# Kernel tuning notes

Hardware: AMD Instinct MI355X
Metric: run time of the kernel (lower is better)

Reference implementation:

```python
import jax, jax.numpy as jnp
import numpy as np
from jax.scipy.special import logsumexp

K, D, H, A = 8, 512, 512, 1024
S, T = 64, 128
B = S * T


def setup_inputs() -> dict:
    key = jax.random.key(0)
    k1, k2, k3, k4 = jax.random.split(key, 4)
    obs = jax.random.normal(k1, (B, D), dtype=jnp.float32)
    actions = jax.random.randint(k2, (B,), 0, A, dtype=jnp.int64)
    # uniform mixture prior (log(1/K)) => all components supported
    start_mixture_logprobs = jnp.full((S, K), jnp.log(1.0 / K), dtype=jnp.float32)
    W1 = jax.random.normal(k3, (K, D, H), dtype=jnp.float32) * 0.02
    b1 = jnp.zeros((K, H), dtype=jnp.float32)
    W2 = jax.random.normal(k4, (K, H, A), dtype=jnp.float32) * 0.02
    b2 = jnp.zeros((K, A), dtype=jnp.float32)
    return {"obs": obs, "actions": actions,
            "start_mixture_logprobs": start_mixture_logprobs,
            "W1": W1, "b1": b1, "W2": W2, "b2": b2, "seq_len": T}


def reference(obs, actions, start_mixture_logprobs, W1, b1, W2, b2, seq_len):
    num_seqs, num_comp = start_mixture_logprobs.shape
    batch = obs.shape[0]
    t_len = batch // num_seqs  # == seq_len
    num_out = W2.shape[-1]

    # per-component MLP on the full batch (all components supported)
    h = jax.nn.relu(jnp.einsum('bd,kdh->kbh', obs, W1) + b1[:, None, :])
    logits = jnp.einsum('kbh,kha->kba', h, W2) + b2[:, None, :]  # [K,B,A]
    component_logprobs = jax.nn.log_softmax(logits, axis=2)      # [K,B,A]

    # add time dimension: [B, K, A] -> [S, T, K, A]
    clp_t = component_logprobs.transpose(1, 0, 2).reshape(num_seqs, t_len, num_comp, num_out)
    act_t = actions.reshape(num_seqs, t_len)

    # gather logprob of taken action per component: [S, T, K]
    idx = jnp.broadcast_to(act_t[:, :, None, None], (num_seqs, t_len, num_comp, 1))
    action_logprobs = jnp.take_along_axis(clp_t, idx, axis=3)[..., 0]
    cum = jnp.cumsum(action_logprobs, axis=1)  # [S,T,K]

    # per-timestep posterior over mixture (shifted cumulative evidence)
    shift = jnp.concatenate([jnp.zeros((num_seqs, 1, num_comp), dtype=cum.dtype), cum[:, :-1]], axis=1)
    mix = jax.nn.log_softmax(start_mixture_logprobs[:, None, :] + shift, axis=2)  # [S,T,K]
    final_mixture_logprobs = jax.nn.log_softmax(start_mixture_logprobs + cum[:, -1], axis=1)

    # combine: logsumexp over components of component_logprobs + mixture logprob
    mix_flat = mix.reshape(batch, num_comp).T  # [K,B]
    model_out = logsumexp(component_logprobs + mix_flat[:, :, None], axis=0)  # [B,A]
    return model_out, final_mixture_logprobs
```

## Files before the change

kernel.cpp:

```cpp
#include <hip/hip_runtime.h>
#include <hip/hip_bf16.h>
#include <stdint.h>

#define KC   8
#define DIM  512
#define HID  512
#define ACTN 1024
#define NS   64
#define NT   128
#define NB   8192
#define PB   8

typedef __attribute__((ext_vector_type(8))) short short8;
typedef __attribute__((ext_vector_type(8))) unsigned short ushort8;
typedef __attribute__((ext_vector_type(4))) float floatx4;
typedef __attribute__((ext_vector_type(2))) float floatx2;
typedef __attribute__((ext_vector_type(4))) unsigned int uint4v;

__device__ inline float bf2f(unsigned short u) {
    return __uint_as_float(((unsigned int)u) << 16);
}
__device__ inline unsigned short f2bf_rne(float x) {
    unsigned int u = __float_as_uint(x);
    u += 0x7fffu + ((u >> 16) & 1u);
    return (unsigned short)(u >> 16);
}

__device__ inline unsigned char f2fp8_manual(float v) {
    unsigned int s = (__float_as_uint(v) >> 24) & 0x80u;
    float a = fabsf(v) * 0x1.0p-120f;
    unsigned int b = __float_as_uint(a);
    b += 0x7FFFFu + ((b >> 20) & 1u);
    unsigned int m = b >> 20;
    if (m > 0x7Eu) m = 0x7Eu;
    return (unsigned char)(s | m);
}
__device__ inline float fp82f_manual(unsigned int byte) {
    unsigned int bits = ((byte & 0x80u) << 24) | ((byte & 0x7Fu) << 20);
    return __uint_as_float(bits) * 0x1.0p+120f;
}
template <bool HI>
__device__ inline unsigned int pk_fp8(float a, float b, unsigned int old) {
#if __has_builtin(__builtin_amdgcn_cvt_pk_fp8_f32)
    return __builtin_amdgcn_cvt_pk_fp8_f32(a, b, old, HI);
#else
    unsigned int p = (unsigned int)f2fp8_manual(a) | ((unsigned int)f2fp8_manual(b) << 8);
    return HI ? ((old & 0x0000ffffu) | (p << 16)) : ((old & 0xffff0000u) | p);
#endif
}
template <bool HI>
__device__ inline floatx2 unpk_fp8(unsigned int src) {
#if __has_builtin(__builtin_amdgcn_cvt_pk_f32_fp8)
    return __builtin_amdgcn_cvt_pk_f32_fp8(src, HI);
#else
    unsigned int w = HI ? (src >> 16) : src;
    floatx2 r;
    r.x = fp82f_manual(w & 0xffu);
    r.y = fp82f_manual((w >> 8) & 0xffu);
    return r;
#endif
}

__device__ inline void gload_lds16(const unsigned short* g, unsigned short* l) {
    __builtin_amdgcn_global_load_lds(
        (const __attribute__((address_space(1))) unsigned int*)g,
        (__attribute__((address_space(3))) unsigned int*)l,
        16, 0, 0);
}

__global__ __launch_bounds__(256) void prep_kernel(
    const float* __restrict__ obs, const float* __restrict__ W1,
    const float* __restrict__ W2,
    unsigned short* __restrict__ obs_bk, unsigned short* __restrict__ W1bk,
    unsigned short* __restrict__ W2bk)
{
    __shared__ float tile[64][65];
    int id = blockIdx.x;
    if (id < 128) {
        int mg = id;
#pragma unroll
        for (int rep = 0; rep < 16; ++rep) {
            int idx = rep * 256 + threadIdx.x;
            int kc  = idx >> 6;
            int row = idx & 63;
            const float* p = obs + ((size_t)(mg * 64 + row) * DIM) + kc * 8;
            ushort8 u;
#pragma unroll
            for (int e = 0; e < 8; e++) u[e] = f2bf_rne(p[e]);
            *(ushort8*)(obs_bk + (((size_t)mg * (DIM / 8) + kc) << 9) + (row << 3)) = u;
        }
        return;
    }
    const float* src; unsigned short* dst; int R, C, xt, yt;
    if (id < 640) {
        int t = id - 128; int z = t >> 6; int rem = t & 63;
        xt = rem & 7; yt = rem >> 3;
        R = DIM; C = HID;
        src = W1 + (size_t)z * DIM * HID; dst = W1bk + (size_t)z * DIM * HID;
    } else {
        int t = id - 640; int z = t >> 7; int rem = t & 127;
        xt = rem & 15; yt = rem >> 4;
        R = HID; C = ACTN;
        src = W2 + (size_t)z * HID * ACTN; dst = W2bk + (size_t)z * HID * ACTN;
    }
    int h0 = xt * 64, d0 = yt * 64;
    int tx = threadIdx.x & 63, ty = threadIdx.x >> 6;
#pragma unroll
    for (int i = 0; i < 64; i += 4)
        tile[ty + i][tx] = src[(size_t)(d0 + ty + i) * C + h0 + tx];
    __syncthreads();
    int KCHR = R >> 3;
#pragma unroll
    for (int rep = 0; rep < 2; ++rep) {
        int idx  = rep * 256 + threadIdx.x;
        int h_l  = idx & 63;
        int dc_l = idx >> 6;
        ushort8 u;
#pragma unroll
        for (int e = 0; e < 8; e++) u[e] = f2bf_rne(tile[dc_l * 8 + e][h_l]);
        size_t off = ((((size_t)(h0 >> 6) * KCHR) + (d0 >> 3) + dc_l) << 9) + (h_l << 3);
        *(ushort8*)(dst + off) = u;
    }
}

__global__ __launch_bounds__(256, 4) void gemm_blk_kernel(
    const unsigned short* __restrict__ Aall,
    const unsigned short* __restrict__ Ball,
    const float* __restrict__ biasall,
    void* __restrict__ Call,
    const int* __restrict__ actions,
    float* __restrict__ psum, float* __restrict__ palp,
    int M, int N, int Kd,
    long long zsA, long long zsB,
    int strideBias, long long strideCbytes,
    int do_relu, int do_lse, int do_blocked)
{
    __shared__ __align__(16) unsigned short S[17408];
    unsigned short* const As = S;
    unsigned short* const Bs = S + 8192;

    const int zb = blockIdx.z;
    const float* bias = biasall + (size_t)zb * strideBias;
    char* const Cbase = (char*)Call + (size_t)zb * strideCbytes;

    const int tid  = threadIdx.x;
    const int lane = tid & 63;
    const int wave = tid >> 6;
    const int wm = wave >> 1;
    const int wn = wave & 1;
    const int quad = lane >> 4;
    const int l16  = lane & 15;

    const int bm = blockIdx.x * 128;
    const int bn = blockIdx.y * 128;
    const int KCH = Kd >> 3;

    floatx4 acc[4][4];
#pragma unroll
    for (int i = 0; i < 4; i++)
#pragma unroll
        for (int j = 0; j < 4; j++)
            acc[i][j] = (floatx4){0.f, 0.f, 0.f, 0.f};

    const int loff = lane << 3;
    const unsigned short* pA = Aall + (size_t)zb * zsA + (((size_t)(bm >> 6) * KCH + wave) << 9) + loff;
    const unsigned short* pB = Ball + (size_t)zb * zsB + (((size_t)(bn >> 6) * KCH + wave) << 9) + loff;
    const size_t mgs = (size_t)KCH << 9;
    unsigned short* ldsA = As + wave * 1024;
    unsigned short* ldsB = Bs + wave * 1024;

    const int nk = Kd >> 6;
    for (int it = 0; it < nk; ++it) {
        __syncthreads();
        gload_lds16(pA,              ldsA);
        gload_lds16(pA + mgs,        ldsA + 512);
        gload_lds16(pA + 2048,       ldsA + 4096);
        gload_lds16(pA + 2048 + mgs, ldsA + 4096 + 512);
        gload_lds16(pB,              ldsB);
        gload_lds16(pB + mgs,        ldsB + 512);
        gload_lds16(pB + 2048,       ldsB + 4096);
        gload_lds16(pB + 2048 + mgs, ldsB + 4096 + 512);
        pA += 4096; pB += 4096;
        __syncthreads();

#pragma unroll
        for (int h = 0; h < 2; ++h) {
            const unsigned short* Ah = As + h * 4096 + quad * 1024;
            const unsigned short* Bh = Bs + h * 4096 + quad * 1024;
            short8 af[4], bfr[4];
#pragma unroll
            for (int i = 0; i < 4; i++)
                af[i] = *(const short8*)(Ah + ((wm * 64 + i * 16 + l16) << 3));
#pragma unroll
            for (int j = 0; j < 4; j++)
                bfr[j] = *(const short8*)(Bh + ((wn * 64 + j * 16 + l16) << 3));
#pragma unroll
            for (int i = 0; i < 4; i++)
#pragma unroll
                for (int j = 0; j < 4; j++)
                    acc[i][j] = __builtin_amdgcn_mfma_f32_16x16x32_bf16(
                        af[i], bfr[j], acc[i][j], 0, 0, 0);
        }
    }
    __syncthreads();

    unsigned short* const Cs = S;
#pragma unroll
    for (int j = 0; j < 4; j++) {
        int col = wn * 64 + j * 16 + l16;
        float bv = bias[bn + col];
#pragma unroll
        for (int i = 0; i < 4; i++) {
            int rw = wm * 64 + i * 16 + quad * 4;
#pragma unroll
            for (int r = 0; r < 4; r++) {
                float v = acc[i][j][r] + bv;
                if (do_relu) v = fmaxf(v, 0.f);
                Cs[(rw + r) * 136 + col] = f2bf_rne(v);
            }
        }
    }
    __syncthreads();

    if (do_blocked) {
        unsigned short* Cb16 = (unsigned short*)Cbase;
        const int KCHo = N >> 3;
#pragma unroll
        for (int rep = 0; rep < 8; ++rep) {
            int idx  = rep * 256 + tid;
            int kc_l = idx >> 7;
            int row  = idx & 127;
            ushort8 u = *(const ushort8*)&Cs[row * 136 + kc_l * 8];
            size_t off = ((((size_t)((bm >> 6) + (row >> 6)) * KCHo) + (bn >> 3) + kc_l) << 9)
                       + ((row & 63) << 3);
            *(ushort8*)(Cb16 + off) = u;
        }
    } else {
        unsigned char* Cb8 = (unsigned char*)Cbase;
        const int row = tid >> 1;
        const int ch  = (tid & 1) * 64;
        unsigned char* crow = Cb8 + (size_t)(bm + row) * N + bn + ch;

        float s = 0.f;
#pragma unroll
        for (int g = 0; g < 4; g++) {
            ushort8 u0 = *(const ushort8*)&Cs[row * 136 + ch + 16 * g];
            ushort8 u1 = *(const ushort8*)&Cs[row * 136 + ch + 16 * g + 8];
            float v[16];
#pragma unroll
            for (int e = 0; e < 8; e++) { v[e] = bf2f(u0[e]); v[8 + e] = bf2f(u1[e]); }
#pragma unroll
            for (int e = 0; e < 16; e++) s += __expf(v[e]);
            uint4v pk;
            pk.x = pk_fp8<true>(v[2],  v[3],  pk_fp8<false>(v[0],  v[1],  0u));
            pk.y = pk_fp8<true>(v[6],  v[7],  pk_fp8<false>(v[4],  v[5],  0u));
            pk.z = pk_fp8<true>(v[10], v[11], pk_fp8<false>(v[8],  v[9],  0u));
            pk.w = pk_fp8<true>(v[14], v[15], pk_fp8<false>(v[12], v[13], 0u));
            *(uint4v*)(crow + 16 * g) = pk;
        }

        float stot = s + __shfl_xor(s, 1);
        size_t kb = (size_t)zb * M + bm + row;
        if ((tid & 1) == 0)
            psum[kb * PB + blockIdx.y] = stot;
        int act = actions[bm + row];
        int rel = act - bn;
        if (rel >= ch && rel < ch + 64)
            palp[kb] = bf2f(Cs[row * 136 + rel]);
    }
}

__global__ __launch_bounds__(128) void mix_kernel(
    const float* __restrict__ palp,
    const float* __restrict__ psum,
    const float* __restrict__ start,
    float* __restrict__ w,
    float* __restrict__ fmix)
{
    __shared__ float buf[2][NT][9];
    int s = blockIdx.x, t = threadIdx.x;
    int b = s * NT + t;

    float a[KC], lsev[KC];
#pragma unroll
    for (int k = 0; k < KC; k++) {
        size_t kb = (size_t)k * NB + b;
        const float* ps = psum + kb * PB;
        float S = 0.f;
#pragma unroll
        for (int p = 0; p < PB; p++) S += ps[p];
        float l = __logf(S);
        lsev[k] = l;
        a[k] = palp[kb] - l;
    }

#pragma unroll
    for (int k = 0; k < KC; k++) buf[0][t][k] = a[k];
    int p = 0;
    for (int off = 1; off < NT; off <<= 1) {
        __syncthreads();
#pragma unroll
        for (int k = 0; k < KC; k++) {
            float x = buf[p][t][k];
            if (t >= off) x += buf[p][t - off][k];
            buf[1 - p][t][k] = x;
        }
        p ^= 1;
    }
    __syncthreads();
    float st[KC], e[KC];
#pragma unroll
    for (int k = 0; k < KC; k++) st[k] = start[s * KC + k];
#pragma unroll
    for (int k = 0; k < KC; k++) e[k] = st[k] + buf[p][t][k] - a[k];
    float m = e[0];
#pragma unroll
    for (int k = 1; k < KC; k++) m = fmaxf(m, e[k]);
    float sum = 0.f;
#pragma unroll
    for (int k = 0; k < KC; k++) sum += __expf(e[k] - m);
    float l = m + __logf(sum);
#pragma unroll
    for (int k = 0; k < KC; k++)
        w[(size_t)k * NB + b] = (e[k] - l) - lsev[k];

    if (t == NT - 1) {
        float f[KC];
#pragma unroll
        for (int k = 0; k < KC; k++) f[k] = st[k] + buf[p][t][k];
        float m2 = f[0];
#pragma unroll
        for (int k = 1; k < KC; k++) m2 = fmaxf(m2, f[k]);
        float s2 = 0.f;
#pragma unroll
        for (int k = 0; k < KC; k++) s2 += __expf(f[k] - m2);
        float l2 = m2 + __logf(s2);
#pragma unroll
        for (int k = 0; k < KC; k++) fmix[s * KC + k] = f[k] - l2;
    }
}

__global__ __launch_bounds__(256) void combine_kernel(
    const unsigned char* __restrict__ logits8,
    const float* __restrict__ w,
    float* __restrict__ out)
{
    int b  = blockIdx.x * 2 + (threadIdx.x >> 7);
    int a0 = (threadIdx.x & 127) * 8;
    float x[KC][8];
#pragma unroll
    for (int k = 0; k < KC; k++) {
        float wv = w[(size_t)k * NB + b];
        uint2 q = *(const uint2*)(logits8 + ((size_t)k * NB + b) * ACTN + a0);
        floatx2 p01 = unpk_fp8<false>(q.x), p23 = unpk_fp8<true>(q.x);
        floatx2 p45 = unpk_fp8<false>(q.y), p67 = unpk_fp8<true>(q.y);
        x[k][0] = p01.x + wv; x[k][1] = p01.y + wv;
        x[k][2] = p23.x + wv; x[k][3] = p23.y + wv;
        x[k][4] = p45.x + wv; x[k][5] = p45.y + wv;
        x[k][6] = p67.x + wv; x[k][7] = p67.y + wv;
    }
    float* op = out + (size_t)b * ACTN + a0;
#pragma unroll
    for (int j = 0; j < 8; j++) {
        float m = x[0][j];
#pragma unroll
        for (int k = 1; k < KC; k++) m = fmaxf(m, x[k][j]);
        float s = 0.f;
#pragma unroll
        for (int k = 0; k < KC; k++) s += __expf(x[k][j] - m);
        op[j] = m + __logf(s);
    }
}

extern "C" void kernel_launch(void* const* d_in, const int* in_sizes, int n_in,
                              void* d_out, int out_size, void* d_ws, size_t ws_size,
                              hipStream_t stream)
{
    const float* obs     = (const float*)d_in[0];
    const int*   actions = (const int*)d_in[1];
    const float* start   = (const float*)d_in[2];
    const float* W1      = (const float*)d_in[3];
    const float* b1      = (const float*)d_in[4];
    const float* W2      = (const float*)d_in[5];
    const float* b2      = (const float*)d_in[6];

    char* ws = (char*)d_ws;
    unsigned short* obs_bk  = (unsigned short*)ws; ws += (size_t)NB * DIM * 2;
    unsigned short* W1bk    = (unsigned short*)ws; ws += (size_t)KC * HID * DIM * 2;
    unsigned short* W2bk    = (unsigned short*)ws; ws += (size_t)KC * ACTN * HID * 2;
    unsigned short* hbuf    = (unsigned short*)ws; ws += (size_t)KC * NB * HID * 2;
    unsigned char*  logits8 = (unsigned char*)ws;  ws += (size_t)KC * NB * ACTN;
    float* wbuf = (float*)ws; ws += (size_t)KC * NB * 4;
    float* psum = (float*)ws; ws += (size_t)KC * NB * PB * 4;
    float* palp = (float*)ws; ws += (size_t)KC * NB * 4;

    float* out  = (float*)d_out;
    float* fmix = out + (size_t)NB * ACTN;

    prep_kernel<<<1664, 256, 0, stream>>>(obs, W1, W2, obs_bk, W1bk, W2bk);

    gemm_blk_kernel<<<dim3(NB / 128, HID / 128, KC), 256, 0, stream>>>(
        obs_bk, W1bk, b1, hbuf, actions, psum, palp,
        NB, HID, DIM,
        0LL, (long long)HID * DIM,
        HID, (long long)NB * HID * 2, 1, 0, 1);

    gemm_blk_kernel<<<dim3(NB / 128, ACTN / 128, KC), 256, 0, stream>>>(
        hbuf, W2bk, b2, logits8, actions, psum, palp,
        NB, ACTN, HID,
        (long long)NB * HID, (long long)ACTN * HID,
        ACTN, (long long)NB * ACTN, 0, 1, 0);

    mix_kernel<<<NS, NT, 0, stream>>>(palp, psum, start, wbuf, fmix);

    combine_kernel<<<NB / 2, 256, 0, stream>>>(logits8, wbuf, out);
}
```

Before: 260.4 us.

## Rewrite GEMM as 256x256 tile, 8-wave, double-buffered pipeline with swizzled LDS layout

The bf16 MFMA GEMM moves from 128x128 tiles with 4 waves and a single LDS buffer to 256x256 tiles with 8 waves. LDS is double-buffered, and global-to-LDS prefetch of the next K-step is interleaved with MFMA phases using explicit barriers, waitcnt and setprio. The blocked layout of the inputs and intermediates becomes 256-row panels with an XOR swizzle to avoid LDS bank conflicts, and the prep kernel is changed to match. The goals are more data reuse per tile and load/compute overlap. The cost is 128KB of LDS per block, fewer blocks in flight, and a shorter grid (psum partitions drop to 4).

```diff
diff --git a/kernel.cpp b/kernel.cpp
--- a/kernel.cpp
+++ b/kernel.cpp
@@ -9,7 +9,7 @@
 #define NS   64
 #define NT   128
 #define NB   8192
-#define PB   8
+#define PB   4
 
 typedef __attribute__((ext_vector_type(8))) short short8;
 typedef __attribute__((ext_vector_type(8))) unsigned short ushort8;
@@ -68,6 +68,7 @@
         16, 0, 0);
 }
 
+
 __global__ __launch_bounds__(256) void prep_kernel(
     const float* __restrict__ obs, const float* __restrict__ W1,
     const float* __restrict__ W2,
@@ -81,13 +82,16 @@
 #pragma unroll
         for (int rep = 0; rep < 16; ++rep) {
             int idx = rep * 256 + threadIdx.x;
-            int kc  = idx >> 6;
-            int row = idx & 63;
-            const float* p = obs + ((size_t)(mg * 64 + row) * DIM) + kc * 8;
+            int row = mg * 64 + (idx >> 6);
+            int c_all = idx & 63;
+            int kt = c_all >> 3, c = c_all & 7;
+            const float* p = obs + (size_t)row * DIM + c_all * 8;
             ushort8 u;
 #pragma unroll
             for (int e = 0; e < 8; e++) u[e] = f2bf_rne(p[e]);
-            *(ushort8*)(obs_bk + (((size_t)mg * (DIM / 8) + kc) << 9) + (row << 3)) = u;
+            size_t off = (((size_t)(row >> 8) * (DIM >> 6) + kt) << 14)
+                       + ((size_t)(row & 255) << 6) + ((c ^ (row & 7)) << 3);
+            *(ushort8*)(obs_bk + off) = u;
         }
         return;
     }
@@ -109,21 +113,22 @@
     for (int i = 0; i < 64; i += 4)
         tile[ty + i][tx] = src[(size_t)(d0 + ty + i) * C + h0 + tx];
     __syncthreads();
-    int KCHR = R >> 3;
 #pragma unroll
     for (int rep = 0; rep < 2; ++rep) {
         int idx  = rep * 256 + threadIdx.x;
         int h_l  = idx & 63;
-        int dc_l = idx >> 6;
+        int dc   = idx >> 6;
+        int rh   = h0 + h_l;
         ushort8 u;
 #pragma unroll
-        for (int e = 0; e < 8; e++) u[e] = f2bf_rne(tile[dc_l * 8 + e][h_l]);
-        size_t off = ((((size_t)(h0 >> 6) * KCHR) + (d0 >> 3) + dc_l) << 9) + (h_l << 3);
+        for (int e = 0; e < 8; e++) u[e] = f2bf_rne(tile[dc * 8 + e][h_l]);
+        size_t off = (((size_t)(rh >> 8) * (R >> 6) + (d0 >> 6)) << 14)
+                   + ((size_t)(rh & 255) << 6) + ((dc ^ (rh & 7)) << 3);
         *(ushort8*)(dst + off) = u;
     }
 }
 
-__global__ __launch_bounds__(256, 4) void gemm_blk_kernel(
+__global__ __launch_bounds__(512, 2) void gemm_blk_kernel(
     const unsigned short* __restrict__ Aall,
     const unsigned short* __restrict__ Ball,
     const float* __restrict__ biasall,
@@ -133,11 +138,9 @@
     int M, int N, int Kd,
     long long zsA, long long zsB,
     int strideBias, long long strideCbytes,
-    int do_relu, int do_lse, int do_blocked)
+    int do_relu, int do_blocked)
 {
-    __shared__ __align__(16) unsigned short S[17408];
-    unsigned short* const As = S;
-    unsigned short* const Bs = S + 8192;
+    __shared__ __align__(16) unsigned short S[65536];
 
     const int zb = blockIdx.z;
     const float* bias = biasall + (size_t)zb * strideBias;
@@ -145,128 +148,177 @@
 
     const int tid  = threadIdx.x;
     const int lane = tid & 63;
-    const int wave = tid >> 6;
-    const int wm = wave >> 1;
-    const int wn = wave & 1;
+    const int w    = tid >> 6;
+    const int wm   = w >> 2;
+    const int wn   = w & 3;
     const int quad = lane >> 4;
     const int l16  = lane & 15;
 
-    const int bm = blockIdx.x * 128;
-    const int bn = blockIdx.y * 128;
-    const int KCH = Kd >> 3;
-
-    floatx4 acc[4][4];
-#pragma unroll
-    for (int i = 0; i < 4; i++)
+    const int bm = blockIdx.x * 256;
+    const int bn = blockIdx.y * 256;
+    const int KT = Kd >> 6;
+    const int nk = KT;
+
+    floatx4 acc[8][4];
+#pragma unroll
+    for (int i = 0; i < 8; i++)
 #pragma unroll
         for (int j = 0; j < 4; j++)
             acc[i][j] = (floatx4){0.f, 0.f, 0.f, 0.f};
 
-    const int loff = lane << 3;
-    const unsigned short* pA = Aall + (size_t)zb * zsA + (((size_t)(bm >> 6) * KCH + wave) << 9) + loff;
-    const unsigned short* pB = Ball + (size_t)zb * zsB + (((size_t)(bn >> 6) * KCH + wave) << 9) + loff;
-    const size_t mgs = (size_t)KCH << 9;
-    unsigned short* ldsA = As + wave * 1024;
-    unsigned short* ldsB = Bs + wave * 1024;
-
-    const int nk = Kd >> 6;
-    for (int it = 0; it < nk; ++it) {
-        __syncthreads();
-        gload_lds16(pA,              ldsA);
-        gload_lds16(pA + mgs,        ldsA + 512);
-        gload_lds16(pA + 2048,       ldsA + 4096);
-        gload_lds16(pA + 2048 + mgs, ldsA + 4096 + 512);
-        gload_lds16(pB,              ldsB);
-        gload_lds16(pB + mgs,        ldsB + 512);
-        gload_lds16(pB + 2048,       ldsB + 4096);
-        gload_lds16(pB + 2048 + mgs, ldsB + 4096 + 512);
-        pA += 4096; pB += 4096;
-        __syncthreads();
-
-#pragma unroll
-        for (int h = 0; h < 2; ++h) {
-            const unsigned short* Ah = As + h * 4096 + quad * 1024;
-            const unsigned short* Bh = Bs + h * 4096 + quad * 1024;
-            short8 af[4], bfr[4];
-#pragma unroll
-            for (int i = 0; i < 4; i++)
-                af[i] = *(const short8*)(Ah + ((wm * 64 + i * 16 + l16) << 3));
+    const unsigned short* srcA = Aall + (size_t)zb * zsA
+        + (((size_t)(bm >> 8) * KT) << 14) + w * 1024 + lane * 8;
+    const unsigned short* srcB = Ball + (size_t)zb * zsB
+        + (((size_t)(bn >> 8) * KT) << 14) + w * 1024 + lane * 8;
+
+    auto stageA = [&](int U, int HF) {
+        const unsigned short* g = srcA + U * 16384 + HF * 8192;
+        unsigned short* l = S + (U & 1) * 32768 + HF * 8192 + w * 1024;
+        gload_lds16(g,       l);
+        gload_lds16(g + 512, l + 512);
+    };
+    auto stageB = [&](int U, int HF) {
+        const unsigned short* g = srcB + U * 16384 + HF * 8192;
+        unsigned short* l = S + (U & 1) * 32768 + 16384 + HF * 8192 + w * 1024;
+        gload_lds16(g,       l);
+        gload_lds16(g + 512, l + 512);
+    };
+
+    const int swz  = (quad ^ (l16 & 7)) << 3;
+    const int aoff0 = (wm * 128 + l16) * 64 + swz;
+    const int boff0 = 16384 + (wn * 64 + l16) * 64 + swz;
+
+    stageA(0, 0); stageA(0, 1); stageB(0, 0); stageB(0, 1);
+    if (nk > 1) { stageA(1, 0); stageA(1, 1); }
+    if (nk > 1) asm volatile("s_waitcnt vmcnt(4)" ::: "memory");
+    else        asm volatile("s_waitcnt vmcnt(0)" ::: "memory");
+    __builtin_amdgcn_s_barrier();
+
+    for (int T = 0; T < nk; ++T) {
+        const int bo = (T & 1) * 32768;
+        short8 a0[8], b0[4], a1[8], b1[4];
+#pragma unroll
+        for (int i = 0; i < 8; i++) a0[i] = *(const short8*)(S + bo + aoff0 + i * 1024);
+#pragma unroll
+        for (int j = 0; j < 4; j++) b0[j] = *(const short8*)(S + bo + boff0 + j * 1024);
+        if (T + 1 < nk) stageB(T + 1, 0);
+        __builtin_amdgcn_s_barrier();
+        __builtin_amdgcn_s_setprio(1);
+#pragma unroll
+        for (int i = 0; i < 4; i++)
 #pragma unroll
             for (int j = 0; j < 4; j++)
-                bfr[j] = *(const short8*)(Bh + ((wn * 64 + j * 16 + l16) << 3));
-#pragma unroll
-            for (int i = 0; i < 4; i++)
-#pragma unroll
-                for (int j = 0; j < 4; j++)
-                    acc[i][j] = __builtin_amdgcn_mfma_f32_16x16x32_bf16(
-                        af[i], bfr[j], acc[i][j], 0, 0, 0);
-        }
-    }
-    __syncthreads();
-
-    unsigned short* const Cs = S;
-#pragma unroll
-    for (int j = 0; j < 4; j++) {
-        int col = wn * 64 + j * 16 + l16;
-        float bv = bias[bn + col];
-#pragma unroll
-        for (int i = 0; i < 4; i++) {
-            int rw = wm * 64 + i * 16 + quad * 4;
-#pragma unroll
-            for (int r = 0; r < 4; r++) {
-                float v = acc[i][j][r] + bv;
-                if (do_relu) v = fmaxf(v, 0.f);
-                Cs[(rw + r) * 136 + col] = f2bf_rne(v);
+                acc[i][j] = __builtin_amdgcn_mfma_f32_16x16x32_bf16(a0[i], b0[j], acc[i][j], 0, 0, 0);
+        __builtin_amdgcn_s_setprio(0);
+        __builtin_amdgcn_s_barrier();
+#pragma unroll
+        for (int i = 0; i < 8; i++) a1[i] = *(const short8*)(S + bo + (aoff0 ^ 32) + i * 1024);
+#pragma unroll
+        for (int j = 0; j < 4; j++) b1[j] = *(const short8*)(S + bo + (boff0 ^ 32) + j * 1024);
+        if (T + 1 < nk) stageB(T + 1, 1);
+        __builtin_amdgcn_s_barrier();
+        __builtin_amdgcn_s_setprio(1);
+#pragma unroll
+        for (int i = 4; i < 8; i++)
+#pragma unroll
+            for (int j = 0; j < 4; j++)
+                acc[i][j] = __builtin_amdgcn_mfma_f32_16x16x32_bf16(a0[i], b0[j], acc[i][j], 0, 0, 0);
+        __builtin_amdgcn_s_setprio(0);
+        asm volatile("s_waitcnt lgkmcnt(0)" ::: "memory");
+        __builtin_amdgcn_s_barrier();
+        if (T + 2 < nk) stageA(T + 2, 0);
+        __builtin_amdgcn_s_barrier();
+        __builtin_amdgcn_s_setprio(1);
+#pragma unroll
+        for (int i = 0; i < 4; i++)
+#pragma unroll
+            for (int j = 0; j < 4; j++)
+                acc[i][j] = __builtin_amdgcn_mfma_f32_16x16x32_bf16(a1[i], b1[j], acc[i][j], 0, 0, 0);
+        __builtin_amdgcn_s_setprio(0);
+        __builtin_amdgcn_s_barrier();
+        if (T + 2 < nk) stageA(T + 2, 1);
+        __builtin_amdgcn_s_barrier();
+        __builtin_amdgcn_s_setprio(1);
+#pragma unroll
+        for (int i = 4; i < 8; i++)
+#pragma unroll
+            for (int j = 0; j < 4; j++)
+                acc[i][j] = __builtin_amdgcn_mfma_f32_16x16x32_bf16(a1[i], b1[j], acc[i][j], 0, 0, 0);
+        __builtin_amdgcn_s_setprio(0);
+        if (T < nk - 2)       asm volatile("s_waitcnt vmcnt(4)" ::: "memory");
+        else if (T == nk - 2) asm volatile("s_waitcnt vmcnt(0)" ::: "memory");
+        __builtin_amdgcn_s_barrier();
+    }
+
+    for (int h = 0; h < 2; ++h) {
+        if (wm == h) {
+#pragma unroll
+            for (int j = 0; j < 4; j++) {
+                int col = wn * 64 + j * 16 + l16;
+                float bv = bias[bn + col];
+#pragma unroll
+                for (int i = 0; i < 8; i++) {
+                    int r0 = i * 16 + quad * 4;
+#pragma unroll
+                    for (int r = 0; r < 4; r++) {
+                        float v = acc[i][j][r] + bv;
+                        if (do_relu) v = fmaxf(v, 0.f);
+                        S[(r0 + r) * 264 + col] = f2bf_rne(v);
+                    }
+                }
             }
         }
-    }
-    __syncthreads();
-
-    if (do_blocked) {
-        unsigned short* Cb16 = (unsigned short*)Cbase;
-        const int KCHo = N >> 3;
-#pragma unroll
-        for (int rep = 0; rep < 8; ++rep) {
-            int idx  = rep * 256 + tid;
-            int kc_l = idx >> 7;
-            int row  = idx & 127;
-            ushort8 u = *(const ushort8*)&Cs[row * 136 + kc_l * 8];
-            size_t off = ((((size_t)((bm >> 6) + (row >> 6)) * KCHo) + (bn >> 3) + kc_l) << 9)
-                       + ((row & 63) << 3);
-            *(ushort8*)(Cb16 + off) = u;
+        __builtin_amdgcn_s_barrier();
+        if (do_blocked) {
+            unsigned short* Cb16 = (unsigned short*)Cbase;
+            const int KTo = N >> 6;
+#pragma unroll
+            for (int rep = 0; rep < 8; ++rep) {
+                int idx  = rep * 512 + tid;
+                int r_l  = idx >> 5;
+                int s5   = idx & 31;
+                int kt_l = s5 >> 3, st = s5 & 7;
+                int r    = h * 128 + r_l;
+                int c    = st ^ (r & 7);
+                ushort8 u = *(const ushort8*)&S[r_l * 264 + kt_l * 64 + c * 8];
+                size_t off = (((size_t)(bm >> 8) * KTo + (bn >> 6) + kt_l) << 14)
+                           + ((size_t)r << 6) + (st << 3);
+                *(ushort8*)(Cb16 + off) = u;
+            }
+        } else {
+            unsigned char* Cb8 = (unsigned char*)Cbase;
+            const int r_l = tid >> 2;
+            const int ch  = (tid & 3) * 64;
+            const int r   = h * 128 + r_l;
+            unsigned char* crow = Cb8 + (size_t)(bm + r) * N + bn + ch;
+            float ssum = 0.f;
+#pragma unroll
+            for (int g = 0; g < 4; g++) {
+                ushort8 u0 = *(const ushort8*)&S[r_l * 264 + ch + 16 * g];
+                ushort8 u1 = *(const ushort8*)&S[r_l * 264 + ch + 16 * g + 8];
+                float v[16];
+#pragma unroll
+                for (int e = 0; e < 8; e++) { v[e] = bf2f(u0[e]); v[8 + e] = bf2f(u1[e]); }
+#pragma unroll
+                for (int e = 0; e < 16; e++) ssum += __expf(v[e]);
+                uint4v pk;
+                pk.x = pk_fp8<true>(v[2],  v[3],  pk_fp8<false>(v[0],  v[1],  0u));
+                pk.y = pk_fp8<true>(v[6],  v[7],  pk_fp8<false>(v[4],  v[5],  0u));
+                pk.z = pk_fp8<true>(v[10], v[11], pk_fp8<false>(v[8],  v[9],  0u));
+                pk.w = pk_fp8<true>(v[14], v[15], pk_fp8<false>(v[12], v[13], 0u));
+                *(uint4v*)(crow + 16 * g) = pk;
+            }
+            float t1 = ssum + __shfl_xor(ssum, 1);
+            float stot = t1 + __shfl_xor(t1, 2);
+            size_t kb = (size_t)zb * M + bm + r;
+            if ((tid & 3) == 0)
+                psum[kb * PB + blockIdx.y] = stot;
+            int a_act = actions[bm + r];
+            int rel = a_act - bn;
+            if (rel >= ch && rel < ch + 64)
+                palp[kb] = bf2f(S[r_l * 264 + rel]);
         }
-    } else {
-        unsigned char* Cb8 = (unsigned char*)Cbase;
-        const int row = tid >> 1;
-        const int ch  = (tid & 1) * 64;
-        unsigned char* crow = Cb8 + (size_t)(bm + row) * N + bn + ch;
-
-        float s = 0.f;
-#pragma unroll
-        for (int g = 0; g < 4; g++) {
-            ushort8 u0 = *(const ushort8*)&Cs[row * 136 + ch + 16 * g];
-            ushort8 u1 = *(const ushort8*)&Cs[row * 136 + ch + 16 * g + 8];
-            float v[16];
-#pragma unroll
-            for (int e = 0; e < 8; e++) { v[e] = bf2f(u0[e]); v[8 + e] = bf2f(u1[e]); }
-#pragma unroll
-            for (int e = 0; e < 16; e++) s += __expf(v[e]);
-            uint4v pk;
-            pk.x = pk_fp8<true>(v[2],  v[3],  pk_fp8<false>(v[0],  v[1],  0u));
-            pk.y = pk_fp8<true>(v[6],  v[7],  pk_fp8<false>(v[4],  v[5],  0u));
-            pk.z = pk_fp8<true>(v[10], v[11], pk_fp8<false>(v[8],  v[9],  0u));
-            pk.w = pk_fp8<true>(v[14], v[15], pk_fp8<false>(v[12], v[13], 0u));
-            *(uint4v*)(crow + 16 * g) = pk;
-        }
-
-        float stot = s + __shfl_xor(s, 1);
-        size_t kb = (size_t)zb * M + bm + row;
-        if ((tid & 1) == 0)
-            psum[kb * PB + blockIdx.y] = stot;
-        int act = actions[bm + row];
-        int rel = act - bn;
-        if (rel >= ch && rel < ch + 64)
-            palp[kb] = bf2f(Cs[row * 136 + rel]);
+        __builtin_amdgcn_s_barrier();
     }
 }
 
@@ -286,10 +338,10 @@
     for (int k = 0; k < KC; k++) {
         size_t kb = (size_t)k * NB + b;
         const float* ps = psum + kb * PB;
-        float S = 0.f;
-#pragma unroll
-        for (int p = 0; p < PB; p++) S += ps[p];
-        float l = __logf(S);
+        float Ssum = 0.f;
+#pragma unroll
+        for (int p = 0; p < PB; p++) Ssum += ps[p];
+        float l = __logf(Ssum);
         lsev[k] = l;
         a[k] = palp[kb] - l;
     }
@@ -399,17 +451,17 @@
 
     prep_kernel<<<1664, 256, 0, stream>>>(obs, W1, W2, obs_bk, W1bk, W2bk);
 
-    gemm_blk_kernel<<<dim3(NB / 128, HID / 128, KC), 256, 0, stream>>>(
+    gemm_blk_kernel<<<dim3(NB / 256, HID / 256, KC), 512, 0, stream>>>(
         obs_bk, W1bk, b1, hbuf, actions, psum, palp,
         NB, HID, DIM,
         0LL, (long long)HID * DIM,
-        HID, (long long)NB * HID * 2, 1, 0, 1);
-
-    gemm_blk_kernel<<<dim3(NB / 128, ACTN / 128, KC), 256, 0, stream>>>(
+        HID, (long long)NB * HID * 2, 1, 1);
+
+    gemm_blk_kernel<<<dim3(NB / 256, ACTN / 256, KC), 512, 0, stream>>>(
         hbuf, W2bk, b2, logits8, actions, psum, palp,
         NB, ACTN, HID,
         (long long)NB * HID, (long long)ACTN * HID,
-        ACTN, (long long)NB * ACTN, 0, 1, 0);
+        ACTN, (long long)NB * ACTN, 0, 0);
 
     mix_kernel<<<NS, NT, 0, stream>>>(palp, psum, start, wbuf, fmix);
 
```

Result: slower. 282.6 us (+8.5%).
